# Optimization experiments

Hardware: AMD Instinct MI355X
Metric: run time of the kernel (lower is better)

The kernel has to match this reference:

```python
import jax, jax.numpy as jnp
import numpy as np
import math

STAGE_NUM = 5
EPS = 1e-6

def _l2norm(a, axis):
    return a / (EPS + jnp.linalg.norm(a, axis=axis, keepdims=True))

def setup_inputs() -> dict:
    key = jax.random.key(0)
    k1, k2, k3, k4 = jax.random.split(key, 4)
    b, n, c, h, w, k, out_c = 4, 4, 256, 64, 64, 128, 256
    x = jax.random.normal(k1, (b, c, h, w), dtype=jnp.float32)
    querys = jax.random.normal(k2, (b * n, c, h, w), dtype=jnp.float32)
    # mu init: normal(0, sqrt(2/k)) then l2norm over channel dim
    mu0 = jax.random.normal(k3, (1, c, k), dtype=jnp.float32) * math.sqrt(2.0 / k)
    mu0 = _l2norm(mu0, axis=1)
    # conv weight: normal(0, sqrt(2/(kh*kw*out_c)))
    fan = 3 * 3 * out_c
    conv_w = jax.random.normal(k4, (out_c, 2 * c, 3, 3), dtype=jnp.float32) * math.sqrt(2.0 / fan)
    conv_b = jnp.zeros((out_c,), dtype=jnp.float32)
    return {"x": x, "querys": querys, "mu0": mu0, "conv_w": conv_w, "conv_b": conv_b, "n": n}

def reference(x, querys, mu0, conv_w, conv_b, n):
    b, c, h, w = x.shape
    k = mu0.shape[2]
    xf = x.reshape(b, c, h * w)                       # [b, c, L]
    mu = jnp.broadcast_to(mu0, (b, c, k))

    # EM iterations (torch.no_grad -> stop_gradient)
    def em_step(mu, _):
        z = jnp.einsum('bcl,bck->blk', xf, mu)        # [b, L, k]
        z = jax.nn.softmax(z, axis=2)
        z_ = z / (EPS + jnp.sum(z, axis=1, keepdims=True))
        mu = jnp.einsum('bcl,blk->bck', xf, z_)       # [b, c, k]
        mu = _l2norm(mu, axis=1)
        return mu, None
    mu, _ = jax.lax.scan(em_step, mu, None, length=STAGE_NUM)
    mu = jax.lax.stop_gradient(mu)

    org_query = querys                                 # [b*n, c, h, w]
    q = querys.reshape(b, n, c, h, w).transpose(0, 2, 1, 3, 4).reshape(b, c, n * h * w)
    q_z = jax.nn.softmax(jnp.einsum('bcl,bck->blk', q, mu), axis=2)  # [b, nL, k]
    q_z = jax.lax.stop_gradient(q_z)

    rec = jnp.einsum('bck,blk->bcl', mu, q_z)          # [b, c, n*h*w]
    rec = rec.reshape(b, c, n, h, w).transpose(0, 2, 1, 3, 4).reshape(b * n, c, h, w)

    cat = jnp.concatenate((org_query, rec), axis=1)    # [b*n, 2c, h, w]
    out = jax.lax.conv_general_dilated(
        cat, conv_w, window_strides=(1, 1), padding='SAME',
        dimension_numbers=('NCHW', 'OIHW', 'NCHW'))
    out = out + conv_b[None, :, None, None]
    return (out, mu)
```

## Files before the change

### kernel.cpp

```cpp
#include <hip/hip_runtime.h>
#include <hip/hip_bf16.h>

#define B   4
#define NN  4
#define C   256
#define HH  64
#define WW  64
#define L   4096
#define NL  16384
#define K   128
#define OC  256
#define IC2 512
#define EPSV 1e-6f
#define PW  66
#define PA  4356

typedef __hip_bfloat16 bf16;
typedef __attribute__((ext_vector_type(8))) __bf16 bf16x8;
typedef __attribute__((ext_vector_type(4))) float f32x4;

#define AS1(p) ((const __attribute__((address_space(1))) void*)(p))
#define AS3(p) ((__attribute__((address_space(3))) void*)(p))

__global__ void k_init(const float* __restrict__ mu0, float* __restrict__ mu_f,
                       bf16* __restrict__ mub) {
    int i = blockIdx.x * 256 + threadIdx.x;
    int rem = i & 32767;
    int k = rem >> 8, c = rem & 255;
    float v = mu0[c * 128 + k];
    mu_f[i] = v;
    mub[i]  = __float2bfloat16(v);
}

__global__ void k_prepx(const float* __restrict__ x, bf16* __restrict__ xb,
                        bf16* __restrict__ xt) {
    __shared__ float ld[64][65];
    int lt = blockIdx.x, ct = blockIdx.y, b = blockIdx.z;
    int t = threadIdx.x;
    #pragma unroll
    for (int i = 0; i < 16; i++) {
        int idx = t + i * 256;
        int ch = idx >> 6, xl = idx & 63;
        size_t a = ((size_t)b * C + ct * 64 + ch) * L + lt * 64 + xl;
        float v = x[a];
        ld[ch][xl] = v;
        xb[a] = __float2bfloat16(v);
    }
    __syncthreads();
    #pragma unroll
    for (int i = 0; i < 16; i++) {
        int idx = t + i * 256;
        int xl = idx >> 6, ch = idx & 63;
        xt[((size_t)b * L + lt * 64 + xl) * 256 + ct * 64 + ch] = __float2bfloat16(ld[ch][xl]);
    }
}

__global__ void k_prepq(const float* __restrict__ qy, bf16* __restrict__ P2) {
    __shared__ float ld[64][65];
    int y = blockIdx.x, ct = blockIdx.y, img = blockIdx.z;
    int t = threadIdx.x;
    #pragma unroll
    for (int i = 0; i < 16; i++) {
        int idx = t + i * 256;
        int ch = idx >> 6, xl = idx & 63;
        ld[ch][xl] = qy[((size_t)img * C + ct * 64 + ch) * L + y * WW + xl];
    }
    __syncthreads();
    #pragma unroll
    for (int i = 0; i < 16; i++) {
        int idx = t + i * 256;
        int xl = idx >> 6, ch = idx & 63;
        P2[((size_t)img * PA + (size_t)(y + 1) * PW + xl + 1) * 512 + ct * 64 + ch] =
            __float2bfloat16(ld[ch][xl]);
    }
}

__global__ void k_zborder(uint4* __restrict__ P2) {
    int pi = blockIdx.x, img = blockIdx.y, t = threadIdx.x;
    int y, x;
    if      (pi < 66)  { y = 0;        x = pi; }
    else if (pi < 132) { y = 65;       x = pi - 66; }
    else if (pi < 196) { y = pi - 131; x = 0; }
    else               { y = pi - 195; x = 65; }
    P2[((size_t)img * PA + (size_t)y * PW + x) * 64 + t] = uint4{0, 0, 0, 0};
}

__global__ void k_wprep(const float* __restrict__ cw, bf16* __restrict__ wb) {
    int idx = blockIdx.x * 256 + threadIdx.x;
    if (idx >= 9 * OC * IC2) return;
    int r  = idx / (OC * IC2);
    int oc = (idx / IC2) & 255;
    int ic = idx & 511;
    wb[idx] = __float2bfloat16(cw[((size_t)oc * IC2 + ic) * 9 + r]);
}

__global__ void __launch_bounds__(256) k_z(const bf16* __restrict__ xt,
                                           const bf16* __restrict__ mub,
                                           bf16* __restrict__ zt) {
    __shared__ __align__(16) char smem[12288];
    char* tA = smem;
    char* tB = smem + 8192;
    int t = threadIdx.x, w = t >> 6, lane = t & 63;
    int b = blockIdx.y, l0 = blockIdx.x * 64;
    const bf16* Ab = mub + (size_t)b * K * C;
    const bf16* Bb = xt + ((size_t)b * L + l0) * C;
    int srow = t >> 2, sseg = t & 3, aseg = sseg ^ (srow & 3);
    char* dA0 = tA + w * 1024;
    char* dA1 = tA + 4096 + w * 1024;
    char* dB  = tB + w * 1024;
    int aoff[8], boff;
    #pragma unroll
    for (int i = 0; i < 8; i++) {
        int rowA = i * 16 + (lane & 15);
        aoff[i] = rowA * 64 + (((lane >> 4) ^ (rowA & 3)) << 4);
    }
    { int rowB = w * 16 + (lane & 15);
      boff = rowB * 64 + (((lane >> 4) ^ (rowB & 3)) << 4); }
    f32x4 acc[8];
    #pragma unroll
    for (int i = 0; i < 8; i++) acc[i] = f32x4{0.f, 0.f, 0.f, 0.f};
    for (int s = 0; s < 8; s++) {
        int cb0 = s * 32 + aseg * 8;
        __syncthreads();
        __builtin_amdgcn_global_load_lds(AS1(Ab + (size_t)srow * C + cb0),        AS3(dA0), 16, 0, 0);
        __builtin_amdgcn_global_load_lds(AS1(Ab + (size_t)(srow + 64) * C + cb0), AS3(dA1), 16, 0, 0);
        __builtin_amdgcn_global_load_lds(AS1(Bb + (size_t)srow * C + cb0),        AS3(dB),  16, 0, 0);
        __syncthreads();
        bf16x8 bfr = *(bf16x8*)(tB + boff);
        #pragma unroll
        for (int i = 0; i < 8; i++) {
            bf16x8 af = *(bf16x8*)(tA + aoff[i]);
            acc[i] = __builtin_amdgcn_mfma_f32_16x16x32_bf16(af, bfr, acc[i], 0, 0, 0);
        }
    }
    float m = -1e30f;
    #pragma unroll
    for (int i = 0; i < 8; i++)
        #pragma unroll
        for (int r = 0; r < 4; r++) m = fmaxf(m, acc[i][r]);
    m = fmaxf(m, __shfl_xor(m, 16, 64));
    m = fmaxf(m, __shfl_xor(m, 32, 64));
    float ssum = 0.f;
    #pragma unroll
    for (int i = 0; i < 8; i++)
        #pragma unroll
        for (int r = 0; r < 4; r++) { acc[i][r] = __expf(acc[i][r] - m); ssum += acc[i][r]; }
    ssum += __shfl_xor(ssum, 16, 64);
    ssum += __shfl_xor(ssum, 32, 64);
    float inv = 1.f / ssum;
    int quad = lane >> 4, col = lane & 15;
    bf16* zb = zt + (size_t)b * K * L + l0 + w * 16 + col;
    #pragma unroll
    for (int i = 0; i < 8; i++)
        #pragma unroll
        for (int r = 0; r < 4; r++) {
            int k = i * 16 + quad * 4 + r;
            zb[(size_t)k * L] = __float2bfloat16(acc[i][r] * inv);
        }
}

__global__ void __launch_bounds__(256) k_mu(const bf16* __restrict__ zt,
                                            const bf16* __restrict__ xb,
                                            float* __restrict__ part) {
    __shared__ __align__(16) char smem[16384];
    char* tA = smem; char* tB = smem + 8192;
    int t = threadIdx.x, w = t >> 6, lane = t & 63;
    int ct = blockIdx.x, chunk = blockIdx.y, b = blockIdx.z;
    const bf16* Ab = zt + (size_t)b * K * L + chunk * 256;
    const bf16* Bb = xb + ((size_t)b * C + ct * 128) * L + chunk * 256;
    int srow = t >> 2, sseg = t & 3, aseg = sseg ^ (srow & 3);
    char* dA0 = tA + w * 1024; char* dA1 = tA + 4096 + w * 1024;
    char* dB0 = tB + w * 1024; char* dB1 = tB + 4096 + w * 1024;
    int wm = w >> 1, wn = w & 1;
    int aoff[4], boff[4];
    #pragma unroll
    for (int i = 0; i < 4; i++) {
        int rowA = wm * 64 + i * 16 + (lane & 15);
        aoff[i] = rowA * 64 + (((lane >> 4) ^ (rowA & 3)) << 4);
        int rowB = wn * 64 + i * 16 + (lane & 15);
        boff[i] = rowB * 64 + (((lane >> 4) ^ (rowB & 3)) << 4);
    }
    f32x4 acc[4][4];
    #pragma unroll
    for (int i = 0; i < 4; i++)
        #pragma unroll
        for (int j = 0; j < 4; j++) acc[i][j] = f32x4{0.f, 0.f, 0.f, 0.f};
    for (int s = 0; s < 8; s++) {
        int lb = s * 32 + aseg * 8;
        __syncthreads();
        __builtin_amdgcn_global_load_lds(AS1(Ab + (size_t)srow * L + lb),        AS3(dA0), 16, 0, 0);
        __builtin_amdgcn_global_load_lds(AS1(Ab + (size_t)(srow + 64) * L + lb), AS3(dA1), 16, 0, 0);
        __builtin_amdgcn_global_load_lds(AS1(Bb + (size_t)srow * L + lb),        AS3(dB0), 16, 0, 0);
        __builtin_amdgcn_global_load_lds(AS1(Bb + (size_t)(srow + 64) * L + lb), AS3(dB1), 16, 0, 0);
        __syncthreads();
        bf16x8 af[4], bfr[4];
        #pragma unroll
        for (int i = 0; i < 4; i++) af[i]  = *(bf16x8*)(tA + aoff[i]);
        #pragma unroll
        for (int j = 0; j < 4; j++) bfr[j] = *(bf16x8*)(tB + boff[j]);
        #pragma unroll
        for (int i = 0; i < 4; i++)
            #pragma unroll
            for (int j = 0; j < 4; j++)
                acc[i][j] = __builtin_amdgcn_mfma_f32_16x16x32_bf16(af[i], bfr[j], acc[i][j], 0, 0, 0);
    }
    float* pb = part + ((size_t)(b * 16 + chunk) * K) * C + ct * 128;
    int quad = lane >> 4, col = lane & 15;
    #pragma unroll
    for (int i = 0; i < 4; i++) {
        int k = wm * 64 + i * 16 + quad * 4;
        #pragma unroll
        for (int j = 0; j < 4; j++) {
            int c = wn * 64 + j * 16 + col;
            #pragma unroll
            for (int r = 0; r < 4; r++)
                pb[(size_t)(k + r) * C + c] = acc[i][j][r];
        }
    }
}

__global__ void k_norm(const float* __restrict__ part, float* __restrict__ mu_f,
                       bf16* __restrict__ mub, bf16* __restrict__ muT) {
    int b = blockIdx.x >> 7, k = blockIdx.x & 127, lane = threadIdx.x;
    float v[4] = {0.f, 0.f, 0.f, 0.f};
    for (int ch = 0; ch < 16; ch++) {
        const float* p = part + ((size_t)(b * 16 + ch) * K + k) * C;
        #pragma unroll
        for (int j = 0; j < 4; j++) v[j] += p[lane + j * 64];
    }
    float s = v[0]*v[0] + v[1]*v[1] + v[2]*v[2] + v[3]*v[3];
    for (int o = 32; o > 0; o >>= 1) s += __shfl_xor(s, o, 64);
    float r = 1.f / (EPSV + sqrtf(s));
    float* mf = mu_f + ((size_t)b * K + k) * C;
    bf16*  mb = mub  + ((size_t)b * K + k) * C;
    bf16*  mt = muT  + (size_t)b * C * K + k;
    #pragma unroll
    for (int j = 0; j < 4; j++) {
        float val = v[j] * r;
        int c = lane + j * 64;
        mf[c] = val;
        mb[c] = __float2bfloat16(val);
        mt[(size_t)c * K] = __float2bfloat16(val);
    }
}

__global__ void __launch_bounds__(256) k_qz(const bf16* __restrict__ P2,
                                            const bf16* __restrict__ mub,
                                            bf16* __restrict__ qz) {
    __shared__ __align__(16) char smem[12288];
    char* tA = smem;
    char* tB = smem + 4096;
    int t = threadIdx.x, w = t >> 6, lane = t & 63;
    int b = blockIdx.y, tile = blockIdx.x;
    int n = tile >> 6, y = tile & 63;
    int img = b * NN + n;
    const bf16* Ab = P2 + ((size_t)img * PA + (size_t)(y + 1) * PW + 1) * 512;
    const bf16* Bb = mub + (size_t)b * K * C;
    int srow = t >> 2, sseg = t & 3, aseg = sseg ^ (srow & 3);
    char* dA  = tA + w * 1024;
    char* dB0 = tB + w * 1024;
    char* dB1 = tB + 4096 + w * 1024;
    int boff[8], aoff;
    #pragma unroll
    for (int j = 0; j < 8; j++) {
        int rowB = j * 16 + (lane & 15);
        boff[j] = rowB * 64 + (((lane >> 4) ^ (rowB & 3)) << 4);
    }
    { int rowA = w * 16 + (lane & 15);
      aoff = rowA * 64 + (((lane >> 4) ^ (rowA & 3)) << 4); }
    f32x4 acc[8];
    #pragma unroll
    for (int j = 0; j < 8; j++) acc[j] = f32x4{0.f, 0.f, 0.f, 0.f};
    for (int s = 0; s < 8; s++) {
        int cb0 = s * 32 + aseg * 8;
        __syncthreads();
        __builtin_amdgcn_global_load_lds(AS1(Ab + (size_t)srow * 512 + cb0),      AS3(dA),  16, 0, 0);
        __builtin_amdgcn_global_load_lds(AS1(Bb + (size_t)srow * C + cb0),        AS3(dB0), 16, 0, 0);
        __builtin_amdgcn_global_load_lds(AS1(Bb + (size_t)(srow + 64) * C + cb0), AS3(dB1), 16, 0, 0);
        __syncthreads();
        bf16x8 af = *(bf16x8*)(tA + aoff);
        #pragma unroll
        for (int j = 0; j < 8; j++) {
            bf16x8 bfr = *(bf16x8*)(tB + boff[j]);
            acc[j] = __builtin_amdgcn_mfma_f32_16x16x32_bf16(af, bfr, acc[j], 0, 0, 0);
        }
    }
    int quad = lane >> 4, col = lane & 15;
    bf16* qb = qz + ((size_t)b * NL + n * L + y * WW + w * 16 + quad * 4) * K;
    #pragma unroll
    for (int r = 0; r < 4; r++) {
        float mm = acc[0][r];
        #pragma unroll
        for (int j = 1; j < 8; j++) mm = fmaxf(mm, acc[j][r]);
        mm = fmaxf(mm, __shfl_xor(mm, 1, 64));
        mm = fmaxf(mm, __shfl_xor(mm, 2, 64));
        mm = fmaxf(mm, __shfl_xor(mm, 4, 64));
        mm = fmaxf(mm, __shfl_xor(mm, 8, 64));
        float ss = 0.f;
        float e[8];
        #pragma unroll
        for (int j = 0; j < 8; j++) { e[j] = __expf(acc[j][r] - mm); ss += e[j]; }
        ss += __shfl_xor(ss, 1, 64);
        ss += __shfl_xor(ss, 2, 64);
        ss += __shfl_xor(ss, 4, 64);
        ss += __shfl_xor(ss, 8, 64);
        float inv = 1.f / ss;
        #pragma unroll
        for (int j = 0; j < 8; j++)
            qb[(size_t)r * K + j * 16 + col] = __float2bfloat16(e[j] * inv);
    }
}

__global__ void __launch_bounds__(256) k_rec(const bf16* __restrict__ qz,
                                             const bf16* __restrict__ muT,
                                             bf16* __restrict__ P2) {
    __shared__ __align__(16) char smem[16384];
    char* tA = smem; char* tB = smem + 8192;
    int t = threadIdx.x, w = t >> 6, lane = t & 63;
    int ct = blockIdx.x, lt = blockIdx.y, b = blockIdx.z;
    const bf16* Ab = qz + ((size_t)b * NL + lt * 128) * K;
    const bf16* Bb = muT + ((size_t)b * C + ct * 128) * K;
    int srow = t >> 2, sseg = t & 3, aseg = sseg ^ (srow & 3);
    char* dA0 = tA + w * 1024; char* dA1 = tA + 4096 + w * 1024;
    char* dB0 = tB + w * 1024; char* dB1 = tB + 4096 + w * 1024;
    int wm = w >> 1, wn = w & 1;
    int aoff[4], boff[4];
    #pragma unroll
    for (int i = 0; i < 4; i++) {
        int rowA = wm * 64 + i * 16 + (lane & 15);
        aoff[i] = rowA * 64 + (((lane >> 4) ^ (rowA & 3)) << 4);
        int rowB = wn * 64 + i * 16 + (lane & 15);
        boff[i] = rowB * 64 + (((lane >> 4) ^ (rowB & 3)) << 4);
    }
    f32x4 acc[4][4];
    #pragma unroll
    for (int i = 0; i < 4; i++)
        #pragma unroll
        for (int j = 0; j < 4; j++) acc[i][j] = f32x4{0.f, 0.f, 0.f, 0.f};
    for (int s = 0; s < 4; s++) {
        int kb = s * 32 + aseg * 8;
        __syncthreads();
        __builtin_amdgcn_global_load_lds(AS1(Ab + (size_t)srow * K + kb),        AS3(dA0), 16, 0, 0);
        __builtin_amdgcn_global_load_lds(AS1(Ab + (size_t)(srow + 64) * K + kb), AS3(dA1), 16, 0, 0);
        __builtin_amdgcn_global_load_lds(AS1(Bb + (size_t)srow * K + kb),        AS3(dB0), 16, 0, 0);
        __builtin_amdgcn_global_load_lds(AS1(Bb + (size_t)(srow + 64) * K + kb), AS3(dB1), 16, 0, 0);
        __syncthreads();
        bf16x8 af[4], bfr[4];
        #pragma unroll
        for (int i = 0; i < 4; i++) af[i]  = *(bf16x8*)(tA + aoff[i]);
        #pragma unroll
        for (int j = 0; j < 4; j++) bfr[j] = *(bf16x8*)(tB + boff[j]);
        #pragma unroll
        for (int i = 0; i < 4; i++)
            #pragma unroll
            for (int j = 0; j < 4; j++)
                acc[i][j] = __builtin_amdgcn_mfma_f32_16x16x32_bf16(af[i], bfr[j], acc[i][j], 0, 0, 0);
    }
    int quad = lane >> 4, col = lane & 15;
    #pragma unroll
    for (int i = 0; i < 4; i++) {
        int lbase = lt * 128 + wm * 64 + i * 16 + quad * 4;
        #pragma unroll
        for (int r = 0; r < 4; r++) {
            int l = lbase + r;
            int n = l >> 12, p = l & 4095;
            int y = p >> 6, xp = p & 63;
            bf16* dst = P2 + ((size_t)(b * NN + n) * PA + (size_t)(y + 1) * PW + xp + 1) * 512 + 256;
            #pragma unroll
            for (int j = 0; j < 4; j++)
                dst[ct * 128 + wn * 64 + j * 16 + col] = __float2bfloat16(acc[i][j][r]);
        }
    }
}

__global__ void __launch_bounds__(256) k_conv(const bf16* __restrict__ P2,
                                              const bf16* __restrict__ Wb,
                                              const float* __restrict__ cb,
                                              float* __restrict__ out) {
    __shared__ __align__(16) char smem[58368];
    char* inl = smem;
    char* wld = smem + 33792;
    int t = threadIdx.x, w = t >> 6, lane = t & 63;
    int m0  = blockIdx.x * 128;
    int y0  = blockIdx.y * 2;
    int img = blockIdx.z;
    int srow = t >> 2, aseg = (t & 3) ^ (srow & 3);
    int wm = w >> 1, wn = w & 1;
    int q = lane >> 4, lane15 = lane & 15, lane7 = lane & 7;

    int aoff[4];
    #pragma unroll
    for (int i = 0; i < 4; i++) {
        int rowA = wm * 64 + i * 16 + lane15;
        aoff[i] = rowA * 64 + ((q ^ (rowA & 3)) << 4);
    }
    int pj[4];
    #pragma unroll
    for (int j = 0; j < 4; j++) pj[j] = wn * 8448 + (j * 16 + lane15) * 128;

    auto stageIN = [&](int cc) {
        #pragma unroll
        for (int rr = 0; rr < 4; rr++) {
            size_t rb = ((size_t)img * PA + (size_t)(y0 + rr) * PW) * 512 + cc * 64;
            #pragma unroll
            for (int hf = 0; hf < 2; hf++) {
                int px = hf * 32 + w * 8 + (lane >> 3);
                int sg = lane7 ^ (px & 7);
                __builtin_amdgcn_global_load_lds(AS1(P2 + rb + (size_t)px * 512 + sg * 8),
                    AS3(inl + rr * 8448 + hf * 4096 + w * 1024), 16, 0, 0);
            }
            if (t < 16) {
                int px = 64 + (lane >> 3);
                int sg = lane7 ^ (px & 7);
                __builtin_amdgcn_global_load_lds(AS1(P2 + rb + (size_t)px * 512 + sg * 8),
                    AS3(inl + rr * 8448 + 8192), 16, 0, 0);
            }
        }
    };

    f32x4 acc[4][4];
    #pragma unroll
    for (int i = 0; i < 4; i++) {
        int oc = m0 + wm * 64 + i * 16 + q * 4;
        #pragma unroll
        for (int r = 0; r < 4; r++) {
            float bv = cb[oc + r];
            #pragma unroll
            for (int j = 0; j < 4; j++) acc[i][j][r] = bv;
        }
    }

    stageIN(0);
    {
        const bf16* w0 = Wb + (size_t)(m0 + srow) * IC2 + aseg * 8;
        __builtin_amdgcn_global_load_lds(AS1(w0),                       AS3(wld + w * 1024), 16, 0, 0);
        __builtin_amdgcn_global_load_lds(AS1(w0 + (size_t)64 * IC2),    AS3(wld + 4096 + w * 1024), 16, 0, 0);
        __builtin_amdgcn_global_load_lds(AS1(w0 + 32),                  AS3(wld + 8192 + w * 1024), 16, 0, 0);
        __builtin_amdgcn_global_load_lds(AS1(w0 + 32 + (size_t)64 * IC2), AS3(wld + 8192 + 4096 + w * 1024), 16, 0, 0);
    }
    asm volatile("s_waitcnt vmcnt(0)" ::: "memory");
    __builtin_amdgcn_s_barrier();
    asm volatile("" ::: "memory");

    for (int cc = 0; cc < 8; cc++) {
        #pragma unroll
        for (int rt = 0; rt < 9; rt++) {
            const int dy = rt / 3, dx = rt % 3;
            #pragma unroll
            for (int h = 0; h < 2; h++) {
                const int STEP = rt * 2 + h;
                char* wb = wld + (STEP % 3) * 8192;
                bf16x8 af[4], bfr[4];
                #pragma unroll
                for (int i = 0; i < 4; i++) af[i] = *(bf16x8*)(wb + aoff[i]);
                int xr  = (((h * 4 + q) ^ ((lane7 + dx) & 7)) << 4);
                int dof = dy * 8448 + dx * 128 + xr;
                #pragma unroll
                for (int j = 0; j < 4; j++) bfr[j] = *(bf16x8*)(inl + pj[j] + dof);
                __builtin_amdgcn_s_setprio(1);
                #pragma unroll
                for (int i = 0; i < 4; i++)
                    #pragma unroll
                    for (int j = 0; j < 4; j++)
                        acc[i][j] = __builtin_amdgcn_mfma_f32_16x16x32_bf16(af[i], bfr[j], acc[i][j], 0, 0, 0);
                __builtin_amdgcn_s_setprio(0);
                const bool wrap = (STEP >= 16);
                bool doPf = (!wrap) || (cc < 7);
                if (doPf) {
                    const int s2 = wrap ? (STEP + 2 - 18) : (STEP + 2);
                    const int r2 = s2 >> 1, h2 = s2 & 1;
                    int cc2 = cc + (wrap ? 1 : 0);
                    char* wdst = wld + ((STEP + 2) % 3) * 8192;
                    const bf16* wsrc = Wb + (size_t)r2 * (OC * IC2) + (size_t)(m0 + srow) * IC2
                                     + cc2 * 64 + h2 * 32 + aseg * 8;
                    __builtin_amdgcn_global_load_lds(AS1(wsrc),                    AS3(wdst + w * 1024), 16, 0, 0);
                    __builtin_amdgcn_global_load_lds(AS1(wsrc + (size_t)64 * IC2), AS3(wdst + 4096 + w * 1024), 16, 0, 0);
                }
                if (STEP == 17) {
                    if (cc < 7) {
                        asm volatile("" ::: "memory");
                        __builtin_amdgcn_s_barrier();
                        asm volatile("" ::: "memory");
                        stageIN(cc + 1);
                        asm volatile("s_waitcnt vmcnt(0)" ::: "memory");
                        __builtin_amdgcn_s_barrier();
                        asm volatile("" ::: "memory");
                    }
                } else {
                    if (doPf) asm volatile("s_waitcnt vmcnt(2)" ::: "memory");
                    else      asm volatile("s_waitcnt vmcnt(0)" ::: "memory");
                    __builtin_amdgcn_s_barrier();
                    asm volatile("" ::: "memory");
                }
            }
        }
    }

    int pxbase = blockIdx.y * 128 + wn * 64 + lane15;
    #pragma unroll
    for (int i = 0; i < 4; i++) {
        int oc = m0 + wm * 64 + i * 16 + q * 4;
        #pragma unroll
        for (int j = 0; j < 4; j++) {
            int px = pxbase + j * 16;
            #pragma unroll
            for (int r = 0; r < 4; r++)
                out[((size_t)img * OC + oc + r) * L + px] = acc[i][j][r];
        }
    }
}

__global__ void k_muout(const float* __restrict__ mu_f, float* __restrict__ out) {
    int i = blockIdx.x * 256 + threadIdx.x;
    int b = i >> 15, rem = i & 32767;
    int c = rem >> 7, k = rem & 127;
    out[(size_t)16777216 + i] = mu_f[((size_t)b * K + k) * C + c];
}

extern "C" void kernel_launch(void* const* d_in, const int* in_sizes, int n_in,
                              void* d_out, int out_size, void* d_ws, size_t ws_size,
                              hipStream_t stream) {
    const float* x   = (const float*)d_in[0];
    const float* qy  = (const float*)d_in[1];
    const float* mu0 = (const float*)d_in[2];
    const float* cw  = (const float*)d_in[3];
    const float* cb  = (const float*)d_in[4];
    float* out = (float*)d_out;

    char* ws = (char*)d_ws;
    float* mu_f = (float*)(ws);
    bf16*  mu_b = (bf16*) (ws + 524288);
    bf16*  muT  = (bf16*) (ws + 786432);
    bf16*  Wb   = (bf16*) (ws + 1048576);
    bf16*  zt   = (bf16*) (ws + 3407872);
    bf16*  qz   = (bf16*) (ws + 3407872);
    bf16*  P2   = (bf16*) (ws + 20185088);
    bf16*  x_bf = (bf16*) (ws + 20185088);
    float* part = (float*)(ws + 20185088 + 8388608);
    bf16*  xt   = (bf16*) (ws + 20185088 + 16777216);

    k_init<<<512, 256, 0, stream>>>(mu0, mu_f, mu_b);
    k_prepx<<<dim3(64, 4, 4), 256, 0, stream>>>(x, x_bf, xt);

    for (int it = 0; it < 5; it++) {
        k_z<<<dim3(64, 4), 256, 0, stream>>>(xt, mu_b, zt);
        k_mu<<<dim3(2, 16, 4), 256, 0, stream>>>(zt, x_bf, part);
        k_norm<<<512, 64, 0, stream>>>(part, mu_f, mu_b, muT);
    }

    k_prepq<<<dim3(64, 4, 16), 256, 0, stream>>>(qy, P2);
    k_zborder<<<dim3(260, 16), 64, 0, stream>>>((uint4*)P2);
    k_wprep<<<4608, 256, 0, stream>>>(cw, Wb);

    k_qz<<<dim3(256, 4), 256, 0, stream>>>(P2, mu_b, qz);
    k_rec<<<dim3(2, 128, 4), 256, 0, stream>>>(qz, muT, P2);
    k_conv<<<dim3(2, 32, 16), 256, 0, stream>>>(P2, Wb, cb, out);
    k_muout<<<512, 256, 0, stream>>>(mu_f, out);
}
```

Measured before the change: 422.6 us.

## Halve conv input-channel chunk to 32 to shrink LDS and raise occupancy

The conv kernel now stages 32 input channels per chunk instead of 64, across 16 chunks. This halves the input tile in LDS (58KB down to 41KB) and redoes the XOR swizzle for the 64-byte rows. Weight prefetch now moves one 32-channel slice per filter tap. The smaller LDS footprint should allow more resident blocks per CU, at the cost of twice as many input-staging barriers and fewer MFMAs per synchronisation.

```diff
diff --git a/kernel.cpp b/kernel.cpp
--- a/kernel.cpp
+++ b/kernel.cpp
@@ -377,44 +377,42 @@
                                               const bf16* __restrict__ Wb,
                                               const float* __restrict__ cb,
                                               float* __restrict__ out) {
-    __shared__ __align__(16) char smem[58368];
+    __shared__ __align__(16) char smem[41472];
     char* inl = smem;
-    char* wld = smem + 33792;
+    char* wld = smem + 16896;
     int t = threadIdx.x, w = t >> 6, lane = t & 63;
     int m0  = blockIdx.x * 128;
     int y0  = blockIdx.y * 2;
     int img = blockIdx.z;
-    int srow = t >> 2, aseg = (t & 3) ^ (srow & 3);
+    int srow = t >> 2;
+    int aseg = (t & 3) ^ ((srow ^ (srow >> 2)) & 3);
     int wm = w >> 1, wn = w & 1;
-    int q = lane >> 4, lane15 = lane & 15, lane7 = lane & 7;
+    int q = lane >> 4, lane15 = lane & 15;
 
     int aoff[4];
     #pragma unroll
     for (int i = 0; i < 4; i++) {
         int rowA = wm * 64 + i * 16 + lane15;
-        aoff[i] = rowA * 64 + ((q ^ (rowA & 3)) << 4);
-    }
-    int pj[4];
-    #pragma unroll
-    for (int j = 0; j < 4; j++) pj[j] = wn * 8448 + (j * 16 + lane15) * 128;
+        aoff[i] = rowA * 64 + (((q ^ (rowA ^ (rowA >> 2))) & 3) << 4);
+    }
+    int pj0[4];
+    #pragma unroll
+    for (int j = 0; j < 4; j++) pj0[j] = j * 16 + lane15;
 
     auto stageIN = [&](int cc) {
-        #pragma unroll
-        for (int rr = 0; rr < 4; rr++) {
-            size_t rb = ((size_t)img * PA + (size_t)(y0 + rr) * PW) * 512 + cc * 64;
-            #pragma unroll
-            for (int hf = 0; hf < 2; hf++) {
-                int px = hf * 32 + w * 8 + (lane >> 3);
-                int sg = lane7 ^ (px & 7);
-                __builtin_amdgcn_global_load_lds(AS1(P2 + rb + (size_t)px * 512 + sg * 8),
-                    AS3(inl + rr * 8448 + hf * 4096 + w * 1024), 16, 0, 0);
-            }
-            if (t < 16) {
-                int px = 64 + (lane >> 3);
-                int sg = lane7 ^ (px & 7);
-                __builtin_amdgcn_global_load_lds(AS1(P2 + rb + (size_t)px * 512 + sg * 8),
-                    AS3(inl + rr * 8448 + 8192), 16, 0, 0);
-            }
+        size_t rowb = ((size_t)img * PA + (size_t)(y0 + w) * PW) * 512 + cc * 32;
+        #pragma unroll
+        for (int it = 0; it < 4; it++) {
+            int px = it * 16 + (lane >> 2);
+            int sg = (lane & 3) ^ ((px ^ (px >> 1)) & 3);
+            __builtin_amdgcn_global_load_lds(AS1(P2 + rowb + (size_t)px * 512 + sg * 8),
+                AS3(inl + w * 4224 + it * 1024), 16, 0, 0);
+        }
+        if (lane < 8) {
+            int px = 64 + (lane >> 2);
+            int sg = (lane & 3) ^ ((px ^ (px >> 1)) & 3);
+            __builtin_amdgcn_global_load_lds(AS1(P2 + rowb + (size_t)px * 512 + sg * 8),
+                AS3(inl + w * 4224 + 4096), 16, 0, 0);
         }
     };
 
@@ -433,65 +431,63 @@
     stageIN(0);
     {
         const bf16* w0 = Wb + (size_t)(m0 + srow) * IC2 + aseg * 8;
-        __builtin_amdgcn_global_load_lds(AS1(w0),                       AS3(wld + w * 1024), 16, 0, 0);
-        __builtin_amdgcn_global_load_lds(AS1(w0 + (size_t)64 * IC2),    AS3(wld + 4096 + w * 1024), 16, 0, 0);
-        __builtin_amdgcn_global_load_lds(AS1(w0 + 32),                  AS3(wld + 8192 + w * 1024), 16, 0, 0);
-        __builtin_amdgcn_global_load_lds(AS1(w0 + 32 + (size_t)64 * IC2), AS3(wld + 8192 + 4096 + w * 1024), 16, 0, 0);
+        __builtin_amdgcn_global_load_lds(AS1(w0),                         AS3(wld + w * 1024), 16, 0, 0);
+        __builtin_amdgcn_global_load_lds(AS1(w0 + (size_t)64 * IC2),      AS3(wld + 4096 + w * 1024), 16, 0, 0);
+        const bf16* w1 = w0 + (size_t)(OC * IC2);
+        __builtin_amdgcn_global_load_lds(AS1(w1),                         AS3(wld + 8192 + w * 1024), 16, 0, 0);
+        __builtin_amdgcn_global_load_lds(AS1(w1 + (size_t)64 * IC2),      AS3(wld + 8192 + 4096 + w * 1024), 16, 0, 0);
     }
     asm volatile("s_waitcnt vmcnt(0)" ::: "memory");
     __builtin_amdgcn_s_barrier();
     asm volatile("" ::: "memory");
 
-    for (int cc = 0; cc < 8; cc++) {
+    for (int cc = 0; cc < 16; cc++) {
         #pragma unroll
         for (int rt = 0; rt < 9; rt++) {
             const int dy = rt / 3, dx = rt % 3;
-            #pragma unroll
-            for (int h = 0; h < 2; h++) {
-                const int STEP = rt * 2 + h;
-                char* wb = wld + (STEP % 3) * 8192;
-                bf16x8 af[4], bfr[4];
+            char* wbuf = wld + (rt % 3) * 8192;
+            bf16x8 af[4], bfr[4];
+            #pragma unroll
+            for (int i = 0; i < 4; i++) af[i] = *(bf16x8*)(wbuf + aoff[i]);
+            #pragma unroll
+            for (int j = 0; j < 4; j++) {
+                int p = pj0[j] + dx;
+                bfr[j] = *(bf16x8*)(inl + (wn + dy) * 4224 + p * 64 +
+                                    (((q ^ (p ^ (p >> 1))) & 3) << 4));
+            }
+            const bool doPf = (cc * 9 + rt + 2) < 144;
+            if (doPf) {
+                const int g2 = rt + 2;
+                const int rt2 = (g2 >= 9) ? g2 - 9 : g2;
+                const int cc2 = cc + (g2 >= 9 ? 1 : 0);
+                char* wdst = wld + ((rt + 2) % 3) * 8192;
+                const bf16* wsrc = Wb + (size_t)rt2 * (OC * IC2) + (size_t)(m0 + srow) * IC2
+                                 + cc2 * 32 + aseg * 8;
+                __builtin_amdgcn_global_load_lds(AS1(wsrc),                    AS3(wdst + w * 1024), 16, 0, 0);
+                __builtin_amdgcn_global_load_lds(AS1(wsrc + (size_t)64 * IC2), AS3(wdst + 4096 + w * 1024), 16, 0, 0);
+            }
+            __builtin_amdgcn_s_setprio(1);
+            #pragma unroll
+            for (int i = 0; i < 4; i++)
                 #pragma unroll
-                for (int i = 0; i < 4; i++) af[i] = *(bf16x8*)(wb + aoff[i]);
-                int xr  = (((h * 4 + q) ^ ((lane7 + dx) & 7)) << 4);
-                int dof = dy * 8448 + dx * 128 + xr;
-                #pragma unroll
-                for (int j = 0; j < 4; j++) bfr[j] = *(bf16x8*)(inl + pj[j] + dof);
-                __builtin_amdgcn_s_setprio(1);
-                #pragma unroll
-                for (int i = 0; i < 4; i++)
-                    #pragma unroll
-                    for (int j = 0; j < 4; j++)
-                        acc[i][j] = __builtin_amdgcn_mfma_f32_16x16x32_bf16(af[i], bfr[j], acc[i][j], 0, 0, 0);
-                __builtin_amdgcn_s_setprio(0);
-                const bool wrap = (STEP >= 16);
-                bool doPf = (!wrap) || (cc < 7);
-                if (doPf) {
-                    const int s2 = wrap ? (STEP + 2 - 18) : (STEP + 2);
-                    const int r2 = s2 >> 1, h2 = s2 & 1;
-                    int cc2 = cc + (wrap ? 1 : 0);
-                    char* wdst = wld + ((STEP + 2) % 3) * 8192;
-                    const bf16* wsrc = Wb + (size_t)r2 * (OC * IC2) + (size_t)(m0 + srow) * IC2
-                                     + cc2 * 64 + h2 * 32 + aseg * 8;
-                    __builtin_amdgcn_global_load_lds(AS1(wsrc),                    AS3(wdst + w * 1024), 16, 0, 0);
-                    __builtin_amdgcn_global_load_lds(AS1(wsrc + (size_t)64 * IC2), AS3(wdst + 4096 + w * 1024), 16, 0, 0);
-                }
-                if (STEP == 17) {
-                    if (cc < 7) {
-                        asm volatile("" ::: "memory");
-                        __builtin_amdgcn_s_barrier();
-                        asm volatile("" ::: "memory");
-                        stageIN(cc + 1);
-                        asm volatile("s_waitcnt vmcnt(0)" ::: "memory");
-                        __builtin_amdgcn_s_barrier();
-                        asm volatile("" ::: "memory");
-                    }
-                } else {
-                    if (doPf) asm volatile("s_waitcnt vmcnt(2)" ::: "memory");
-                    else      asm volatile("s_waitcnt vmcnt(0)" ::: "memory");
+                for (int j = 0; j < 4; j++)
+                    acc[i][j] = __builtin_amdgcn_mfma_f32_16x16x32_bf16(af[i], bfr[j], acc[i][j], 0, 0, 0);
+            __builtin_amdgcn_s_setprio(0);
+            if (rt == 8) {
+                if (cc < 15) {
+                    asm volatile("" ::: "memory");
+                    __builtin_amdgcn_s_barrier();
+                    asm volatile("" ::: "memory");
+                    stageIN(cc + 1);
+                    asm volatile("s_waitcnt vmcnt(0)" ::: "memory");
                     __builtin_amdgcn_s_barrier();
                     asm volatile("" ::: "memory");
                 }
+            } else {
+                if (doPf) asm volatile("s_waitcnt vmcnt(2)" ::: "memory");
+                else      asm volatile("s_waitcnt vmcnt(0)" ::: "memory");
+                __builtin_amdgcn_s_barrier();
+                asm volatile("" ::: "memory");
             }
         }
     }
```

After: 425.7 us. About the same (+0.7%).
